# Performance work log

Hardware: AMD Instinct MI355X
Metric: run time of the kernel (lower is better)

Reference implementation:

```python
import jax, jax.numpy as jnp
import numpy as np

HEADS = 8
DIM_HEAD = 64
DIM = 512
INNER = HEADS * DIM_HEAD  # 512
SCALE = DIM_HEAD ** -0.5


def setup_inputs() -> dict:
    key = jax.random.key(0)
    k1, k2, k3, k4 = jax.random.split(key, 4)
    B, N = 2, 4096
    x = jax.random.normal(k1, (B, N, DIM), dtype=jnp.float32)
    # nn.Linear(dim, inner*3, bias=False): weight [3*inner, dim]; y = x @ W.T
    w_qkv = jax.random.normal(k2, (3 * INNER, DIM), dtype=jnp.float32) * (DIM ** -0.5)
    w_out = jax.random.normal(k3, (DIM, INNER), dtype=jnp.float32) * (INNER ** -0.5)
    b_out = jax.random.normal(k4, (DIM,), dtype=jnp.float32) * 0.01
    return {"x": x, "w_qkv": w_qkv, "w_out": w_out, "b_out": b_out, "H": 64, "W": 64}


def reference(x, w_qkv, w_out, b_out, H, W):
    B, N, _ = x.shape
    qkv = jnp.einsum('bnd,ed->bne', x, w_qkv)  # [B, N, 3*inner]
    q, k, v = jnp.split(qkv, 3, axis=-1)
    def to_heads(t):
        return t.reshape(B, N, HEADS, DIM_HEAD).transpose(0, 2, 1, 3)  # b h n d
    q, k, v = to_heads(q), to_heads(k), to_heads(v)
    dots = jnp.einsum('bhid,bhjd->bhij', q, k) * SCALE
    attn = jax.nn.softmax(dots, axis=-1)  # dropout p=0.0 -> identity
    out = jnp.einsum('bhij,bhjd->bhid', attn, v)
    out = out.transpose(0, 2, 1, 3).reshape(B, N, INNER)
    return jnp.einsum('bne,de->bnd', out, w_out) + b_out
```

## Files before the change

kernel.cpp:

```cpp
#include <hip/hip_runtime.h>
#include <hip/hip_bf16.h>

typedef __hip_bfloat16 bf16;
typedef __attribute__((ext_vector_type(8))) short short8;
typedef __attribute__((ext_vector_type(4))) short shortx4;
typedef __attribute__((ext_vector_type(4))) float floatx4;
typedef __attribute__((ext_vector_type(4))) int intx4;

#define MFMA16(a, b, c) __builtin_amdgcn_mfma_f32_16x16x32_bf16((a), (b), (c), 0, 0, 0)
#define EXP2(x) __builtin_amdgcn_exp2f(x)

__device__ __forceinline__ short f2s(float v) {
    return __builtin_bit_cast(short, __float2bfloat16(v));
}

__device__ __forceinline__ int packhi(float lo, float hi) {
    return (int)__builtin_amdgcn_perm(__builtin_bit_cast(unsigned, hi),
                                      __builtin_bit_cast(unsigned, lo),
                                      0x07060302u);
}

__device__ __forceinline__ short8 cvt8v(float4 f0, float4 f1) {
    short8 r;
    r[0] = f2s(f0.x); r[1] = f2s(f0.y); r[2] = f2s(f0.z); r[3] = f2s(f0.w);
    r[4] = f2s(f1.x); r[5] = f2s(f1.y); r[6] = f2s(f1.z); r[7] = f2s(f1.w);
    return r;
}

__device__ __forceinline__ int swz(int row, int chunk) {
    return row * 64 + ((chunk ^ (row & 7)) << 3);
}
__device__ __forceinline__ int swzv(int row, int chunk) {
    return row * 128 + ((chunk ^ (row & 7)) << 3);
}
__device__ __forceinline__ int sfun(int r) { return (r + (r >> 2)) & 3; }
__device__ __forceinline__ int swz4(int row, int chunk) {
    return row * 32 + ((chunk ^ sfun(row)) << 3);
}

__device__ __forceinline__ void gload16(const bf16* g, short* l) {
    __builtin_amdgcn_global_load_lds(
        (const __attribute__((address_space(1))) void*)g,
        (__attribute__((address_space(3))) void*)l, 16, 0, 0);
}

__global__ __launch_bounds__(256) void cvt_inputs(
    const float* __restrict__ x, const float* __restrict__ wq,
    const float* __restrict__ wo, bf16* __restrict__ xb,
    bf16* __restrict__ wqb, bf16* __restrict__ wob)
{
    int idx = blockIdx.x * 256 + threadIdx.x;
    const float* src;
    bf16* dst;
    int off;
    if (idx < 524288)      { src = x;  dst = xb;  off = idx; }
    else if (idx < 622592) { src = wq; dst = wqb; off = idx - 524288; }
    else                   { src = wo; dst = wob; off = idx - 622592; }
    float4 f0 = ((const float4*)src)[off * 2];
    float4 f1 = ((const float4*)src)[off * 2 + 1];
    *(short8*)&((short*)dst)[off * 8] = cvt8v(f0, f1);
}

__global__ __launch_bounds__(256) void qkv_gemm(
    const bf16* __restrict__ xb, const bf16* __restrict__ wqb,
    bf16* __restrict__ q, bf16* __restrict__ k, bf16* __restrict__ vt)
{
    __shared__ short pool[20480];
    short* As = pool;
    short* Bs = pool + 8192;
    short (*Qt)[144] = (short(*)[144])pool;
    short (*Vt)[136] = (short(*)[136])pool;
    const int t = threadIdx.x;
    const int n = blockIdx.x;
    const int xcd = n & 7, m = n >> 3;
    const int by = m % 12, bxl = m / 12;
    const int bm = (xcd * 8 + bxl) * 128;
    const int be = by * 128;
    const int w = t >> 6, lane = t & 63, lq = lane >> 4, lm = lane & 15;
    const int wr = w >> 1, wc = w & 1;
    const float C = 0.18033688011112042f;

    const int r0s = t >> 2, c0s = t & 3;
    const int ga0 = (c0s ^ sfun(r0s)) * 8;
    const int ga1 = (c0s ^ sfun(64 + r0s)) * 8;
    const bf16* xp0 = &xb[(size_t)(bm + r0s) * 512 + ga0];
    const bf16* xp1 = &xb[(size_t)(bm + 64 + r0s) * 512 + ga1];
    const bf16* wp0 = &wqb[(size_t)(be + r0s) * 512 + ga0];
    const bf16* wp1 = &wqb[(size_t)(be + 64 + r0s) * 512 + ga1];

    auto stage = [&](int k0, int buf) {
        short* Ab = As + buf * 4096;
        short* Bb = Bs + buf * 4096;
        gload16(xp0 + k0, &Ab[t * 8]);
        gload16(xp1 + k0, &Ab[2048 + t * 8]);
        gload16(wp0 + k0, &Bb[t * 8]);
        gload16(wp1 + k0, &Bb[2048 + t * 8]);
    };

    floatx4 acc[4][4];
#pragma unroll
    for (int i = 0; i < 4; ++i)
#pragma unroll
        for (int j = 0; j < 4; ++j) acc[i][j] = {0.f, 0.f, 0.f, 0.f};

    stage(0, 0);
    __syncthreads();
    int cur = 0;
    for (int k0 = 0; k0 < 512; k0 += 32) {
        const bool more = (k0 + 32) < 512;
        if (more) stage(k0 + 32, cur ^ 1);
        const short* Ab = As + cur * 4096;
        const short* Bb = Bs + cur * 4096;
        short8 af[4], bf[4];
#pragma unroll
        for (int mt = 0; mt < 4; ++mt)
            af[mt] = *(const short8*)&Ab[swz4(wr * 64 + mt * 16 + lm, lq)];
#pragma unroll
        for (int nt = 0; nt < 4; ++nt)
            bf[nt] = *(const short8*)&Bb[swz4(wc * 64 + nt * 16 + lm, lq)];
#pragma unroll
        for (int mt = 0; mt < 4; ++mt)
#pragma unroll
            for (int nt = 0; nt < 4; ++nt)
                acc[mt][nt] = MFMA16(af[mt], bf[nt], acc[mt][nt]);
        __syncthreads();
        cur ^= 1;
    }

    const int which = be >> 9;
    if (which < 2) {
        const float scale = (which == 0) ? C : 1.0f;
#pragma unroll
        for (int nt = 0; nt < 4; ++nt) {
            const int e_loc = wc * 64 + nt * 16 + lm;
#pragma unroll
            for (int mt = 0; mt < 4; ++mt)
#pragma unroll
                for (int r = 0; r < 4; ++r)
                    Qt[wr * 64 + mt * 16 + lq * 4 + r][e_loc] = f2s(acc[mt][nt][r] * scale);
        }
        __syncthreads();
        bf16* dst = (which == 0) ? q : k;
        const int tr = t >> 1, th = t & 1;
        const int grow = bm + tr;
        const int b = grow >> 12, nn = grow & 4095;
        const int h = ((be + th * 64) & 511) >> 6;
        bf16* p = dst + ((size_t)(b * 8 + h) * 4096 + nn) * 64;
#pragma unroll
        for (int c = 0; c < 8; ++c)
            *(intx4*)&p[c * 8] = *(const intx4*)&Qt[tr][th * 64 + c * 8];
    } else {
#pragma unroll
        for (int nt = 0; nt < 4; ++nt) {
            const int e_loc = wc * 64 + nt * 16 + lm;
#pragma unroll
            for (int mt = 0; mt < 4; ++mt) {
                const int col = wr * 64 + 4 * (mt & 1) + 8 * lq + 32 * (mt >> 1);
                shortx4 v4;
#pragma unroll
                for (int r = 0; r < 4; ++r) v4[r] = f2s(acc[mt][nt][r]);
                *(shortx4*)&Vt[e_loc][col] = v4;
            }
        }
        __syncthreads();
        const int b = bm >> 12, n0 = bm & 4095;
        const int h0 = (be - 1024) >> 6;
        const int row = t >> 1, cb = (t & 1) * 64;
        const int h = h0 + (row >> 6), d = row & 63;
        const size_t gb = ((size_t)(b * 8 + h) * 64 + d) * 4096 + n0 + cb;
#pragma unroll
        for (int c = 0; c < 8; ++c)
            *(intx4*)&vt[gb + c * 8] = *(const intx4*)&Vt[row][cb + c * 8];
    }
}

__global__ __launch_bounds__(256, 2) void flash_attn(
    const bf16* __restrict__ q, const bf16* __restrict__ k,
    const bf16* __restrict__ vt, bf16* __restrict__ out)
{
    __shared__ short pool[40960];
    short* Qs  = pool;
    short* Ks0 = pool + 8192;
    short* Vs0 = pool + 24576;
    const int t = threadIdx.x;
    const int n = blockIdx.x;
    const int L = (n & 7) * 64 + (n >> 3);
    const int i0 = (L & 31) * 128;
    const int bh = L >> 5;
    const int w = t >> 6, lane = t & 63, lq = lane >> 4, lm = lane & 15;
    const int h = w >> 1;
    const int par = w & 1;
    const floatx4 zero4 = {0.f, 0.f, 0.f, 0.f};

    const size_t nbase = (size_t)bh * 4096 * 64;
    const size_t vbase = (size_t)bh * 64 * 4096;
    const int r0 = t >> 3, ch = t & 7;

#pragma unroll
    for (int it = 0; it < 4; ++it) {
        int row = it * 32 + r0;
        *(intx4*)&Qs[swz(row, ch)] =
            *(const intx4*)&q[nbase + (size_t)(i0 + row) * 64 + ch * 8];
    }

    const int kr = t >> 1, kc = (t & 1) * 4;
    const int vr = t >> 2, vc = (t & 3) * 4;
    const bf16* kp0 = &k[nbase + (size_t)kr * 64 + kc * 8];
    const bf16* vp0 = &vt[vbase + (size_t)vr * 4096 + vc * 8];
    int kso[4], vso[4];
#pragma unroll
    for (int c = 0; c < 4; ++c) {
        kso[c] = swz(kr, kc + c);
        vso[c] = swzv(vr, vc + c);
    }

    intx4 kreg[4], vreg[4];
    auto issue = [&](int j0n) {
        const intx4* kp = (const intx4*)(kp0 + (size_t)j0n * 64);
        const intx4* vp = (const intx4*)(vp0 + j0n);
#pragma unroll
        for (int c = 0; c < 4; ++c) { kreg[c] = kp[c]; vreg[c] = vp[c]; }
    };
    auto commit = [&](int buf) {
        short* Kb = Ks0 + buf * 8192;
        short* Vb = Vs0 + buf * 8192;
#pragma unroll
        for (int c = 0; c < 4; ++c) {
            *(intx4*)&Kb[kso[c]] = kreg[c];
            *(intx4*)&Vb[vso[c]] = vreg[c];
        }
    };

    issue(0);
    commit(0);
    __syncthreads();

    short8 aq0[4], aq1[4];
#pragma unroll
    for (int g = 0; g < 4; ++g) {
        const int qrow = h * 64 + g * 16 + lm;
        aq0[g] = *(const short8*)&Qs[swz(qrow, lq)];
        aq1[g] = *(const short8*)&Qs[swz(qrow, 4 + lq)];
    }

    float l_lane[4] = {0.f, 0.f, 0.f, 0.f};
    floatx4 o_acc[4][4];
#pragma unroll
    for (int g = 0; g < 4; ++g)
#pragma unroll
        for (int dt = 0; dt < 4; ++dt) o_acc[g][dt] = zero4;

    const int jtb = par * 4;
    int cur = 0;
    for (int j0 = 0; j0 < 4096; j0 += 128) {
        const bool more = (j0 + 128) < 4096;
        if (more) issue(j0 + 128);
        const short* Kb = Ks0 + cur * 8192;
        const short* Vb = Vs0 + cur * 8192;

        intx4 pkA[4], pkB[4];
#pragma unroll
        for (int q2 = 0; q2 < 4; ++q2) {
            const int krow = (jtb + q2) * 16 + lm;
            short8 bk0 = *(const short8*)&Kb[swz(krow, lq)];
            short8 bk1 = *(const short8*)&Kb[swz(krow, 4 + lq)];
#pragma unroll
            for (int g = 0; g < 4; ++g) {
                floatx4 s4 = MFMA16(bk0, aq0[g], zero4);
                s4 = MFMA16(bk1, aq1[g], s4);
                float e0 = EXP2(s4[0]);
                float e1 = EXP2(s4[1]);
                float e2 = EXP2(s4[2]);
                float e3 = EXP2(s4[3]);
                l_lane[g] += (e0 + e1) + (e2 + e3);
                int p01 = packhi(e0, e1), p23 = packhi(e2, e3);
                if (q2 < 2) { pkA[g][q2 * 2] = p01; pkA[g][q2 * 2 + 1] = p23; }
                else { pkB[g][(q2 - 2) * 2] = p01; pkB[g][(q2 - 2) * 2 + 1] = p23; }
            }
        }

        __builtin_amdgcn_s_setprio(1);
#pragma unroll
        for (int dt = 0; dt < 4; ++dt) {
            const int vrow = dt * 16 + lm;
            short8 av0 = *(const short8*)&Vb[swzv(vrow, par * 8 + lq)];
            short8 av1 = *(const short8*)&Vb[swzv(vrow, par * 8 + 4 + lq)];
#pragma unroll
            for (int g = 0; g < 4; ++g) {
                o_acc[g][dt] = MFMA16(av0, __builtin_bit_cast(short8, pkA[g]), o_acc[g][dt]);
                o_acc[g][dt] = MFMA16(av1, __builtin_bit_cast(short8, pkB[g]), o_acc[g][dt]);
            }
        }
        __builtin_amdgcn_s_setprio(0);

        if (more) {
            commit(cur ^ 1);
            __syncthreads();
        }
        cur ^= 1;
    }

    __syncthreads();
    float* Red = (float*)(pool + 8192);
    float* Lx  = (float*)pool;
    if (par == 1) {
#pragma unroll
        for (int g = 0; g < 4; ++g) {
            Lx[h * 256 + g * 64 + lane] = l_lane[g];
#pragma unroll
            for (int dt = 0; dt < 4; ++dt)
#pragma unroll
                for (int r = 0; r < 4; ++r)
                    Red[h * 4096 + ((g * 4 + dt) * 4 + r) * 64 + lane] = o_acc[g][dt][r];
        }
    }
    __syncthreads();
    if (par == 0) {
        const int b = bh >> 3, hd = bh & 7;
        short* Os = pool + 1024 + h * 1024;
        const int il = lane >> 2, cc = (lane & 3) * 16;
#pragma unroll
        for (int g = 0; g < 4; ++g) {
            float l = l_lane[g] + Lx[h * 256 + g * 64 + lane];
#pragma unroll
            for (int dt = 0; dt < 4; ++dt)
#pragma unroll
                for (int r = 0; r < 4; ++r)
                    o_acc[g][dt][r] += Red[h * 4096 + ((g * 4 + dt) * 4 + r) * 64 + lane];
            l += __shfl_xor(l, 16);
            l += __shfl_xor(l, 32);
            const float inv_l = 1.0f / l;
#pragma unroll
            for (int dt = 0; dt < 4; ++dt)
#pragma unroll
                for (int r = 0; r < 4; ++r)
                    Os[lm * 64 + dt * 16 + lq * 4 + r] = f2s(o_acc[g][dt][r] * inv_l);
            const int i = i0 + h * 64 + g * 16 + il;
            intx4 v0 = *(const intx4*)&Os[il * 64 + cc];
            intx4 v1 = *(const intx4*)&Os[il * 64 + cc + 8];
            *(intx4*)&out[((size_t)b * 4096 + i) * 512 + hd * 64 + cc] = v0;
            *(intx4*)&out[((size_t)b * 4096 + i) * 512 + hd * 64 + cc + 8] = v1;
        }
    }
}

__global__ __launch_bounds__(256) void out_gemm(
    const bf16* __restrict__ a, const bf16* __restrict__ wob,
    const float* __restrict__ bias, float* __restrict__ y)
{
    __shared__ short pool[12288];
    short* As = pool;
    short* Bs = pool + 8192;
    const int t = threadIdx.x;
    const int n = blockIdx.x;
    const int xcd = n & 7, m = n >> 3;
    const int by = m & 7, bxl = m >> 3;
    const int bm = (xcd * 8 + bxl) * 128;
    const int be = by * 64;
    const int w = t >> 6, lane = t & 63, lq = lane >> 4, lm = lane & 15;
    const int wr = w >> 1, wc = w & 1;

    const int r0s = t >> 2, c0s = t & 3;
    const int ga0 = (c0s ^ sfun(r0s)) * 8;
    const int ga1 = (c0s ^ sfun(64 + r0s)) * 8;
    const bf16* ap0 = &a[(size_t)(bm + r0s) * 512 + ga0];
    const bf16* ap1 = &a[(size_t)(bm + 64 + r0s) * 512 + ga1];
    const bf16* wp0 = &wob[(size_t)(be + r0s) * 512 + ga0];

    auto stage = [&](int k0, int buf) {
        short* Ab = As + buf * 4096;
        short* Bb = Bs + buf * 2048;
        gload16(ap0 + k0, &Ab[t * 8]);
        gload16(ap1 + k0, &Ab[2048 + t * 8]);
        gload16(wp0 + k0, &Bb[t * 8]);
    };

    floatx4 acc[4][2];
#pragma unroll
    for (int i = 0; i < 4; ++i)
#pragma unroll
        for (int j = 0; j < 2; ++j) acc[i][j] = {0.f, 0.f, 0.f, 0.f};

    stage(0, 0);
    __syncthreads();
    int cur = 0;
    for (int k0 = 0; k0 < 512; k0 += 32) {
        const bool more = (k0 + 32) < 512;
        if (more) stage(k0 + 32, cur ^ 1);
        const short* Ab = As + cur * 4096;
        const short* Bb = Bs + cur * 2048;
        short8 af[4], bf[2];
#pragma unroll
        for (int mt = 0; mt < 4; ++mt)
            af[mt] = *(const short8*)&Ab[swz4(wr * 64 + mt * 16 + lm, lq)];
#pragma unroll
        for (int nt = 0; nt < 2; ++nt)
            bf[nt] = *(const short8*)&Bb[swz4(wc * 32 + nt * 16 + lm, lq)];
#pragma unroll
        for (int mt = 0; mt < 4; ++mt)
#pragma unroll
            for (int nt = 0; nt < 2; ++nt)
                acc[mt][nt] = MFMA16(af[mt], bf[nt], acc[mt][nt]);
        __syncthreads();
        cur ^= 1;
    }

#pragma unroll
    for (int nt = 0; nt < 2; ++nt) {
        const int gcol = be + wc * 32 + nt * 16 + lm;
        const float bv = bias[gcol];
#pragma unroll
        for (int mt = 0; mt < 4; ++mt) {
#pragma unroll
            for (int r = 0; r < 4; ++r) {
                int grow = bm + wr * 64 + mt * 16 + lq * 4 + r;
                y[(size_t)grow * 512 + gcol] = acc[mt][nt][r] + bv;
            }
        }
    }
}

extern "C" void kernel_launch(void* const* d_in, const int* in_sizes, int n_in,
                              void* d_out, int out_size, void* d_ws, size_t ws_size,
                              hipStream_t stream) {
    const float* x     = (const float*)d_in[0];
    const float* w_qkv = (const float*)d_in[1];
    const float* w_out = (const float*)d_in[2];
    const float* b_out = (const float*)d_in[3];

    const size_t HEAD_ELEMS = (size_t)16 * 4096 * 64;
    bf16* qw  = (bf16*)d_ws;
    bf16* kw  = qw + HEAD_ELEMS;
    bf16* vtw = kw + HEAD_ELEMS;
    bf16* aw  = vtw + HEAD_ELEMS;
    bf16* xb  = aw + HEAD_ELEMS;
    bf16* wqb = xb + (size_t)8192 * 512;
    bf16* wob = wqb + (size_t)1536 * 512;
    float* y  = (float*)d_out;

    cvt_inputs<<<2560, 256, 0, stream>>>(x, w_qkv, w_out, xb, wqb, wob);
    qkv_gemm<<<768, 256, 0, stream>>>(xb, wqb, qw, kw, vtw);
    flash_attn<<<dim3(512), 256, 0, stream>>>(qw, kw, vtw, aw);
    out_gemm<<<512, 256, 0, stream>>>(aw, wob, b_out, y);
}
```

Measured before the change: 187.3 us.

## Fuse fp32-to-bf16 input conversion into the QKV and output GEMM loaders

Removes the separate conversion kernel and its bf16 workspace copies. qkv_gemm now loads fp32 x and w_qkv tiles into registers, converts them and stores them swizzled into LDS, with the next tile's loads issued before the MFMA work. out_gemm does the same for w_out while keeping async LDS loads for the attention output. This saves one launch and an extra global round trip, but doubles the global bytes per GEMM tile read and replaces direct-to-LDS loads with register staging.

```diff
diff --git a/kernel.cpp b/kernel.cpp
--- a/kernel.cpp
+++ b/kernel.cpp
@@ -44,25 +44,8 @@
         (__attribute__((address_space(3))) void*)l, 16, 0, 0);
 }
 
-__global__ __launch_bounds__(256) void cvt_inputs(
+__global__ __launch_bounds__(256) void qkv_gemm(
     const float* __restrict__ x, const float* __restrict__ wq,
-    const float* __restrict__ wo, bf16* __restrict__ xb,
-    bf16* __restrict__ wqb, bf16* __restrict__ wob)
-{
-    int idx = blockIdx.x * 256 + threadIdx.x;
-    const float* src;
-    bf16* dst;
-    int off;
-    if (idx < 524288)      { src = x;  dst = xb;  off = idx; }
-    else if (idx < 622592) { src = wq; dst = wqb; off = idx - 524288; }
-    else                   { src = wo; dst = wob; off = idx - 622592; }
-    float4 f0 = ((const float4*)src)[off * 2];
-    float4 f1 = ((const float4*)src)[off * 2 + 1];
-    *(short8*)&((short*)dst)[off * 8] = cvt8v(f0, f1);
-}
-
-__global__ __launch_bounds__(256) void qkv_gemm(
-    const bf16* __restrict__ xb, const bf16* __restrict__ wqb,
     bf16* __restrict__ q, bf16* __restrict__ k, bf16* __restrict__ vt)
 {
     __shared__ short pool[20480];
@@ -80,21 +63,24 @@
     const int wr = w >> 1, wc = w & 1;
     const float C = 0.18033688011112042f;
 
-    const int r0s = t >> 2, c0s = t & 3;
-    const int ga0 = (c0s ^ sfun(r0s)) * 8;
-    const int ga1 = (c0s ^ sfun(64 + r0s)) * 8;
-    const bf16* xp0 = &xb[(size_t)(bm + r0s) * 512 + ga0];
-    const bf16* xp1 = &xb[(size_t)(bm + 64 + r0s) * 512 + ga1];
-    const bf16* wp0 = &wqb[(size_t)(be + r0s) * 512 + ga0];
-    const bf16* wp1 = &wqb[(size_t)(be + 64 + r0s) * 512 + ga1];
-
-    auto stage = [&](int k0, int buf) {
+    const int srow = t >> 1, scb = (t & 1) * 2;
+    const float* xp = &x[(size_t)(bm + srow) * 512 + scb * 8];
+    const float* wp = &wq[(size_t)(be + srow) * 512 + scb * 8];
+
+    float4 xr[4], wr4[4];
+    auto issue = [&](int k0) {
+        const float4* a = (const float4*)(xp + k0);
+        const float4* b = (const float4*)(wp + k0);
+#pragma unroll
+        for (int c = 0; c < 4; ++c) { xr[c] = a[c]; wr4[c] = b[c]; }
+    };
+    auto commit = [&](int buf) {
         short* Ab = As + buf * 4096;
         short* Bb = Bs + buf * 4096;
-        gload16(xp0 + k0, &Ab[t * 8]);
-        gload16(xp1 + k0, &Ab[2048 + t * 8]);
-        gload16(wp0 + k0, &Bb[t * 8]);
-        gload16(wp1 + k0, &Bb[2048 + t * 8]);
+        *(short8*)&Ab[swz4(srow, scb)]     = cvt8v(xr[0], xr[1]);
+        *(short8*)&Ab[swz4(srow, scb + 1)] = cvt8v(xr[2], xr[3]);
+        *(short8*)&Bb[swz4(srow, scb)]     = cvt8v(wr4[0], wr4[1]);
+        *(short8*)&Bb[swz4(srow, scb + 1)] = cvt8v(wr4[2], wr4[3]);
     };
 
     floatx4 acc[4][4];
@@ -103,12 +89,13 @@
 #pragma unroll
         for (int j = 0; j < 4; ++j) acc[i][j] = {0.f, 0.f, 0.f, 0.f};
 
-    stage(0, 0);
+    issue(0);
+    commit(0);
     __syncthreads();
     int cur = 0;
     for (int k0 = 0; k0 < 512; k0 += 32) {
         const bool more = (k0 + 32) < 512;
-        if (more) stage(k0 + 32, cur ^ 1);
+        if (more) issue(k0 + 32);
         const short* Ab = As + cur * 4096;
         const short* Bb = Bs + cur * 4096;
         short8 af[4], bf[4];
@@ -123,11 +110,15 @@
 #pragma unroll
             for (int nt = 0; nt < 4; ++nt)
                 acc[mt][nt] = MFMA16(af[mt], bf[nt], acc[mt][nt]);
-        __syncthreads();
+        if (more) {
+            commit(cur ^ 1);
+            __syncthreads();
+        }
         cur ^= 1;
     }
 
     const int which = be >> 9;
+    __syncthreads();
     if (which < 2) {
         const float scale = (which == 0) ? C : 1.0f;
 #pragma unroll
@@ -345,7 +336,7 @@
 }
 
 __global__ __launch_bounds__(256) void out_gemm(
-    const bf16* __restrict__ a, const bf16* __restrict__ wob,
+    const bf16* __restrict__ a, const float* __restrict__ wo,
     const float* __restrict__ bias, float* __restrict__ y)
 {
     __shared__ short pool[12288];
@@ -365,14 +356,21 @@
     const int ga1 = (c0s ^ sfun(64 + r0s)) * 8;
     const bf16* ap0 = &a[(size_t)(bm + r0s) * 512 + ga0];
     const bf16* ap1 = &a[(size_t)(bm + 64 + r0s) * 512 + ga1];
-    const bf16* wp0 = &wob[(size_t)(be + r0s) * 512 + ga0];
-
-    auto stage = [&](int k0, int buf) {
+    const float* wp = &wo[(size_t)(be + (t >> 2)) * 512 + (t & 3) * 8];
+    const int bso = swz4(t >> 2, t & 3);
+
+    float4 br0, br1;
+    auto stageA = [&](int k0, int buf) {
         short* Ab = As + buf * 4096;
-        short* Bb = Bs + buf * 2048;
         gload16(ap0 + k0, &Ab[t * 8]);
         gload16(ap1 + k0, &Ab[2048 + t * 8]);
-        gload16(wp0 + k0, &Bb[t * 8]);
+    };
+    auto issueB = [&](int k0) {
+        const float4* b = (const float4*)(wp + k0);
+        br0 = b[0]; br1 = b[1];
+    };
+    auto commitB = [&](int buf) {
+        *(short8*)&Bs[buf * 2048 + bso] = cvt8v(br0, br1);
     };
 
     floatx4 acc[4][2];
@@ -381,12 +379,14 @@
 #pragma unroll
         for (int j = 0; j < 2; ++j) acc[i][j] = {0.f, 0.f, 0.f, 0.f};
 
-    stage(0, 0);
+    stageA(0, 0);
+    issueB(0);
+    commitB(0);
     __syncthreads();
     int cur = 0;
     for (int k0 = 0; k0 < 512; k0 += 32) {
         const bool more = (k0 + 32) < 512;
-        if (more) stage(k0 + 32, cur ^ 1);
+        if (more) { stageA(k0 + 32, cur ^ 1); issueB(k0 + 32); }
         const short* Ab = As + cur * 4096;
         const short* Bb = Bs + cur * 2048;
         short8 af[4], bf[2];
@@ -401,7 +401,10 @@
 #pragma unroll
             for (int nt = 0; nt < 2; ++nt)
                 acc[mt][nt] = MFMA16(af[mt], bf[nt], acc[mt][nt]);
-        __syncthreads();
+        if (more) {
+            commitB(cur ^ 1);
+            __syncthreads();
+        }
         cur ^= 1;
     }
 
@@ -433,13 +436,9 @@
     bf16* kw  = qw + HEAD_ELEMS;
     bf16* vtw = kw + HEAD_ELEMS;
     bf16* aw  = vtw + HEAD_ELEMS;
-    bf16* xb  = aw + HEAD_ELEMS;
-    bf16* wqb = xb + (size_t)8192 * 512;
-    bf16* wob = wqb + (size_t)1536 * 512;
     float* y  = (float*)d_out;
 
-    cvt_inputs<<<2560, 256, 0, stream>>>(x, w_qkv, w_out, xb, wqb, wob);
-    qkv_gemm<<<768, 256, 0, stream>>>(xb, wqb, qw, kw, vtw);
+    qkv_gemm<<<768, 256, 0, stream>>>(x, w_qkv, qw, kw, vtw);
     flash_attn<<<dim3(512), 256, 0, stream>>>(qw, kw, vtw, aw);
-    out_gemm<<<512, 256, 0, stream>>>(aw, wob, b_out, y);
-}
+    out_gemm<<<512, 256, 0, stream>>>(aw, w_out, b_out, y);
+}
```

New measurement: 200.8 us. 7.2% more time.
